# Optimization experiments

Measured on AMD Instinct MI355X. Metric: run time of the kernel, lower is better.

## Reference

```python
import jax, jax.numpy as jnp
import numpy as np

B, S, D, H = 2, 2048, 768, 12
DK = D // H


def setup_inputs() -> dict:
    key = jax.random.key(0)
    ks = jax.random.split(key, 10)
    sc = 0.02
    return {
        "k": jax.random.normal(ks[0], (B, S, D), jnp.float32),
        "q": jax.random.normal(ks[1], (B, S, D), jnp.float32),
        "v": jax.random.normal(ks[2], (B, S, D), jnp.float32),
        "mask": jnp.ones((B, 1, S, S), jnp.int32),
        "wq": jax.random.normal(ks[3], (D, D), jnp.float32) * sc,
        "bq": jnp.zeros((D,), jnp.float32),
        "wk": jax.random.normal(ks[4], (D, D), jnp.float32) * sc,
        "bk": jnp.zeros((D,), jnp.float32),
        "wv": jax.random.normal(ks[5], (D, D), jnp.float32) * sc,
        "bv": jnp.zeros((D,), jnp.float32),
        "wo": jax.random.normal(ks[6], (D, D), jnp.float32) * sc,
        "bo": jnp.zeros((D,), jnp.float32),
    }


def reference(k, q, v, mask, wq, bq, wk, bk, wv, bv, wo, bo):
    # Linear projections (torch Linear: x @ W^T + b)
    query = q @ wq.T + bq
    key_ = k @ wk.T + bk
    value = v @ wv.T + bv
    # [B,S,D] -> [B,H,S,DK]
    def split_heads(x):
        return x.reshape(B, S, H, DK).transpose(0, 2, 1, 3)
    Q, K, V = split_heads(query), split_heads(key_), split_heads(value)
    # NOTE: original masked_fill result is discarded -> mask is a no-op.
    scores = jnp.einsum("bhqd,bhkd->bhqk", Q, K) / jnp.sqrt(jnp.float32(DK))
    attn = jax.nn.softmax(scores, axis=-1)  # dropout p=0.0 -> identity
    out = jnp.einsum("bhqk,bhkd->bhqd", attn, V)
    out = out.transpose(0, 2, 1, 3).reshape(B, S, D)
    return out @ wo.T + bo
```

## Files before the change

### kernel.cpp

```cpp
#include <hip/hip_runtime.h>
#include <hip/hip_bf16.h>

#define B_  2
#define S_  2048
#define D_  768
#define H_  12
#define DK_ 64
#define NX_ (B_*S_*D_)
#define NW_ (D_*D_)
#define CSC 0.18033688011112042f

typedef __attribute__((ext_vector_type(8))) short  bf16x8;
typedef __attribute__((ext_vector_type(4))) float  f32x4;

__device__ __forceinline__ unsigned short f2bf(float f) {
    unsigned int u = __float_as_uint(f);
    u += 0x7fffu + ((u >> 16) & 1u);
    return (unsigned short)(u >> 16);
}

__device__ __forceinline__ unsigned pack_bf2(float a, float b) {
    const unsigned ua = __float_as_uint(a) + 0x8000u;
    const unsigned ub = __float_as_uint(b) + 0x8000u;
    return __builtin_amdgcn_perm(ub, ua, 0x07060302u);
}

__device__ __forceinline__ void async_cp16(const unsigned short* g,
                                           const unsigned short* lds_uniform_base) {
    __builtin_amdgcn_global_load_lds(
        (const __attribute__((address_space(1))) unsigned int*)(uintptr_t)g,
        (__attribute__((address_space(3))) unsigned int*)(unsigned int)(uintptr_t)lds_uniform_base,
        16, 0, 0);
}

struct CvtArgs { const float* s[7]; };

__global__ __launch_bounds__(256) void cvt_all(CvtArgs a,
                                               unsigned short* __restrict__ Xsw,
                                               unsigned short* __restrict__ Wsw) {
    const int bx = blockIdx.x;
    int y, inner;
    if (bx < 2304) { y = bx / 768;             inner = bx % 768; }
    else           { y = 3 + (bx - 2304) / 144; inner = (bx - 2304) % 144; }
    const int idx = inner * 256 + threadIdx.x;
    const int n  = idx / 48;
    const int g2 = idx % 48;
    const float* src = a.s[y] + (long)n * D_ + g2 * 16;
    const float zs = (y == 3) ? CSC : 1.0f;
    unsigned short o[16];
#pragma unroll
    for (int i = 0; i < 4; i++) {
        const float4 f = *(const float4*)(src + i * 4);
        o[i*4+0] = f2bf(f.x*zs); o[i*4+1] = f2bf(f.y*zs);
        o[i*4+2] = f2bf(f.z*zs); o[i*4+3] = f2bf(f.w*zs);
    }
    unsigned short* dst = (y >= 3) ? (Wsw + (long)(y - 3) * NW_ + (long)n * D_)
                                   : (Xsw + (long)y * NX_ + (long)n * D_);
    const int key = n & 7;
#pragma unroll
    for (int h = 0; h < 2; h++) {
        const int g8 = g2 * 2 + h;
        const int kdst = (g8 >> 3) * 64 + (((g8 & 7) ^ key) * 8);
        *(uint4*)(dst + kdst) = *(const uint4*)&o[h * 8];
    }
}

struct QkvArgs { const float* bias[3]; unsigned short* out[3]; };

__global__ __launch_bounds__(256, 3) void gemm_qkv(QkvArgs args,
                                                   const unsigned short* __restrict__ Xsw,
                                                   const unsigned short* __restrict__ Wsw) {
    __shared__ __align__(16) unsigned short smem[17408];
    unsigned short* As = smem;
    unsigned short* Bs = smem + 8192;

    const int t    = threadIdx.x;
    const int wave = t >> 6;
    const int lane = t & 63;
    const int l16  = lane & 15;
    const int quad = lane >> 4;
    const int wm   = wave >> 1, wn = wave & 1;
    const int m0   = blockIdx.x * 128;
    const int zz   = blockIdx.y / 6;
    const int nb   = blockIdx.y % 6;
    const int n0   = nb * 128;

    const unsigned short* Ap = Xsw + (long)zz * NX_;
    const unsigned short* Wp = Wsw + (long)zz * NW_;

    f32x4 acc[4][4];
#pragma unroll
    for (int s = 0; s < 4; s++)
#pragma unroll
        for (int j = 0; j < 4; j++) acc[s][j] = (f32x4){0.f, 0.f, 0.f, 0.f};

    const int lrow = lane >> 3;
    const int lcg  = lane & 7;

    for (int k0 = 0; k0 < D_; k0 += 64) {
        __syncthreads();
#pragma unroll
        for (int i = 0; i < 4; i++) {
            const int chunk = wave * 4 + i;
            async_cp16(Ap + (long)(m0 + chunk * 8 + lrow) * D_ + k0 + lcg * 8,
                       As + chunk * 512);
        }
#pragma unroll
        for (int i = 0; i < 4; i++) {
            const int chunk = wave * 4 + i;
            async_cp16(Wp + (long)(n0 + chunk * 8 + lrow) * D_ + k0 + lcg * 8,
                       Bs + chunk * 512);
        }
        __syncthreads();
#pragma unroll
        for (int ks = 0; ks < 2; ks++) {
            const int cg = ks * 4 + quad;
            bf16x8 af[4], bf[4];
#pragma unroll
            for (int s = 0; s < 4; s++) {
                const int r = wm * 64 + s * 16 + l16;
                af[s] = *(const bf16x8*)&As[r * 64 + ((cg ^ (r & 7)) * 8)];
            }
#pragma unroll
            for (int j = 0; j < 4; j++) {
                const int r = wn * 64 + j * 16 + l16;
                bf[j] = *(const bf16x8*)&Bs[r * 64 + ((cg ^ (r & 7)) * 8)];
            }
#pragma unroll
            for (int s = 0; s < 4; s++)
#pragma unroll
                for (int j = 0; j < 4; j++)
                    acc[s][j] = __builtin_amdgcn_mfma_f32_16x16x32_bf16(af[s], bf[j], acc[s][j], 0, 0, 0);
        }
    }
    __syncthreads();

    const int b     = m0 >> 11;
    const int sbase = m0 & (S_ - 1);
    const float zs  = (zz == 0) ? CSC : 1.0f;
    float bv[4];
#pragma unroll
    for (int j = 0; j < 4; j++) bv[j] = args.bias[zz][n0 + wn * 64 + j * 16 + l16] * zs;

    if (zz < 2) {
        unsigned short* Ls = smem;
#pragma unroll
        for (int s = 0; s < 4; s++)
#pragma unroll
            for (int j = 0; j < 4; j++)
#pragma unroll
                for (int r = 0; r < 4; r++)
                    Ls[(wm * 64 + s * 16 + quad * 4 + r) * 136 + wn * 64 + j * 16 + l16] =
                        f2bf(acc[s][j][r] + bv[j]);
        __syncthreads();
        const int row  = t >> 1;
        const int half = t & 1;
        unsigned short* Op = args.out[zz];
#pragma unroll
        for (int i = 0; i < 8; i++) {
            const int col  = half * 64 + i * 8;
            const int head = nb * 2 + half;
            const uint4 v = *(const uint4*)&Ls[row * 136 + col];
            *(uint4*)(Op + ((long)(b * H_ + head) * S_ + sbase + row) * DK_
                         + ((i ^ (row & 7)) * 8)) = v;
        }
    } else {
        unsigned short* Ls = smem;
#pragma unroll
        for (int s = 0; s < 4; s++)
#pragma unroll
            for (int j = 0; j < 4; j++)
#pragma unroll
                for (int r = 0; r < 4; r++) {
                    const int dk  = j * 16 + l16;
                    const int pos = wm * 64 + (quad * 4 + r) * 4 + s;
                    Ls[wn * 8704 + dk * 136 + pos] = f2bf(acc[s][j][r] + bv[j]);
                }
        __syncthreads();
        const int rowIdx = t >> 1;
        const int hh = rowIdx >> 6, dk = rowIdx & 63;
        const int half = t & 1;
        unsigned short* Op = args.out[2];
#pragma unroll
        for (int i = 0; i < 8; i++) {
            const int col = half * 64 + i * 8;
            const uint4 v = *(const uint4*)&Ls[hh * 8704 + dk * 136 + col];
            const int head = nb * 2 + hh;
            *(uint4*)(Op + ((long)(b * H_ + head) * DK_ + dk) * S_
                         + sbase + half * 64 + ((i ^ (dk & 7)) * 8)) = v;
        }
    }
}

__global__ __launch_bounds__(256, 3) void attn_kernel(
    const unsigned short* __restrict__ Q, const unsigned short* __restrict__ K,
    const unsigned short* __restrict__ Vt, unsigned short* __restrict__ Ao)
{
    const int t    = threadIdx.x;
    const int wave = t >> 6;
    const int lane = t & 63;
    const int l16  = lane & 15;
    const int quad = lane >> 4;
    const int bid  = blockIdx.x;
    const int bh    = bid % 24;
    const int qtile = bid / 24;

    const unsigned short* Qp = Q  + (long)bh * S_ * DK_;
    const unsigned short* Kp = K  + (long)bh * S_ * DK_;
    const unsigned short* Vp = Vt + (long)bh * DK_ * S_;

    __shared__ __align__(16) unsigned short smem[20480];
    unsigned short* Ps = smem + 16384;

    const int fkey = l16 & 7;
    const int fo0  = ((quad ^ fkey) * 8);
    const int fo1  = (((4 + quad) ^ fkey) * 8);

    bf16x8 qfrag[2];
    {
        const long qoff = (long)(qtile * 64 + wave * 16 + l16) * DK_;
        qfrag[0] = *(const bf16x8*)(Qp + qoff + fo0);
        qfrag[1] = *(const bf16x8*)(Qp + qoff + fo1);
    }

    const int ci0 = wave * 2;
    const int kd0 = ci0 * 512;
    const unsigned short* gk  = Kp + ci0 * 512 + lane * 8;
    const unsigned short* gv0 = Vp + (long)(ci0 * 8 + (lane >> 3)) * S_ + (lane & 7) * 8;
    const unsigned short* gv1 = gv0 + 8 * S_;

    async_cp16(gk,        smem + kd0);
    async_cp16(gk + 512,  smem + kd0 + 512);
    async_cp16(gv0,       smem + 8192 + kd0);
    async_cp16(gv1,       smem + 8192 + kd0 + 512);
    gk += 4096;  gv0 += 64;  gv1 += 64;

    f32x4 oacc[4];
#pragma unroll
    for (int j = 0; j < 4; j++) oacc[j] = (f32x4){0.f, 0.f, 0.f, 0.f};
    float lsum[4] = {0.f, 0.f, 0.f, 0.f};

    for (int it = 0; it < 32; ++it) {
        const int co = (it & 1) * 4096;
        const int no = 4096 - co;
        __syncthreads();
        const unsigned short* Ks = smem + co;
        const unsigned short* Vs = smem + 8192 + co;

        if (it < 31) {
            async_cp16(gk,        smem + no + kd0);
            async_cp16(gk + 512,  smem + no + kd0 + 512);
            async_cp16(gv0,       smem + 8192 + no + kd0);
            async_cp16(gv1,       smem + 8192 + no + kd0 + 512);
            gk += 4096;  gv0 += 64;  gv1 += 64;
        }

        f32x4 sacc[4];
#pragma unroll
        for (int j = 0; j < 4; j++) sacc[j] = (f32x4){0.f, 0.f, 0.f, 0.f};
#pragma unroll
        for (int ks = 0; ks < 2; ks++) {
            const int fo = ks ? fo1 : fo0;
            const bf16x8 qf = ks ? qfrag[1] : qfrag[0];
#pragma unroll
            for (int j = 0; j < 4; j++) {
                const bf16x8 bf = *(const bf16x8*)&Ks[(j * 16 + l16) * 64 + fo];
                sacc[j] = __builtin_amdgcn_mfma_f32_16x16x32_bf16(qf, bf, sacc[j], 0, 0, 0);
            }
        }

#pragma unroll
        for (int r = 0; r < 4; r++) {
            const float p0 = exp2f(sacc[0][r]);
            const float p1 = exp2f(sacc[1][r]);
            const float p2 = exp2f(sacc[2][r]);
            const float p3 = exp2f(sacc[3][r]);
            lsum[r] += (p0 + p1) + (p2 + p3);
            uint2 pk = {pack_bf2(p0, p1), pack_bf2(p2, p3)};
            const int prow = wave * 16 + quad * 4 + r;
            *(uint2*)&Ps[prow * 64 + (((l16 >> 1) ^ (prow & 7)) * 8) + (l16 & 1) * 4] = pk;
        }

#pragma unroll
        for (int ks = 0; ks < 2; ks++) {
            const int fo = ks ? fo1 : fo0;
            const bf16x8 pf = *(const bf16x8*)&Ps[(wave * 16 + l16) * 64 + fo];
#pragma unroll
            for (int j = 0; j < 4; j++) {
                const bf16x8 vf = *(const bf16x8*)&Vs[(j * 16 + l16) * 64 + fo];
                oacc[j] = __builtin_amdgcn_mfma_f32_16x16x32_bf16(pf, vf, oacc[j], 0, 0, 0);
            }
        }
    }

#pragma unroll
    for (int r = 0; r < 4; r++) {
#pragma unroll
        for (int off = 1; off < 16; off <<= 1)
            lsum[r] += __shfl_xor(lsum[r], off, 64);
        lsum[r] = 1.f / lsum[r];
    }

    __syncthreads();
#pragma unroll
    for (int j = 0; j < 4; j++)
#pragma unroll
        for (int r = 0; r < 4; r++) {
            const int row = wave * 16 + quad * 4 + r;
            const int c   = j * 2 + (l16 >> 3);
            Ps[row * 64 + ((c ^ (row & 7)) * 8) + (l16 & 7)] =
                f2bf(oacc[j][r] * lsum[r]);
        }

    const int b = bh / H_, h = bh % H_;
    const int row = t >> 2;
    const int p0  = (t & 3) * 2;
    const int qrow = qtile * 64 + row;
    unsigned short* dst = Ao + (long)(b * S_ + qrow) * D_ + h * DK_;
    *(uint4*)(dst + p0 * 8)       = *(const uint4*)&Ps[row * 64 + p0 * 8];
    *(uint4*)(dst + (p0 + 1) * 8) = *(const uint4*)&Ps[row * 64 + (p0 + 1) * 8];
}

__global__ __launch_bounds__(256, 4) void gemm_out(
    const unsigned short* __restrict__ A, const unsigned short* __restrict__ Wsw,
    const float* __restrict__ bias, float* __restrict__ Out)
{
    __shared__ __align__(16) unsigned short smem[8704];
    unsigned short* As = smem;
    unsigned short* Bs = smem + 4096;

    const int t    = threadIdx.x;
    const int wave = t >> 6;
    const int lane = t & 63;
    const int l16  = lane & 15;
    const int quad = lane >> 4;
    const int wm   = wave >> 1, wn = wave & 1;
    const int m0   = blockIdx.x * 64;
    const int n0   = blockIdx.y * 64;

    f32x4 acc[2][2];
#pragma unroll
    for (int s = 0; s < 2; s++)
#pragma unroll
        for (int j = 0; j < 2; j++) acc[s][j] = (f32x4){0.f, 0.f, 0.f, 0.f};

    const int lrow = lane >> 3;
    const int lcg  = lane & 7;

    for (int k0 = 0; k0 < D_; k0 += 64) {
        __syncthreads();
#pragma unroll
        for (int i = 0; i < 2; i++) {
            const int chunk = wave * 2 + i;
            async_cp16(A + (long)(m0 + chunk * 8 + lrow) * D_ + k0 + lcg * 8,
                       As + chunk * 512);
        }
#pragma unroll
        for (int i = 0; i < 2; i++) {
            const int chunk = wave * 2 + i;
            async_cp16(Wsw + (long)(n0 + chunk * 8 + lrow) * D_ + k0 + lcg * 8,
                       Bs + chunk * 512);
        }
        __syncthreads();
#pragma unroll
        for (int ks = 0; ks < 2; ks++) {
            const int cg = ks * 4 + quad;
            bf16x8 af[2], bf[2];
#pragma unroll
            for (int s = 0; s < 2; s++) {
                const int r = wm * 32 + s * 16 + l16;
                af[s] = *(const bf16x8*)&As[r * 64 + ((cg ^ (r & 7)) * 8)];
            }
#pragma unroll
            for (int j = 0; j < 2; j++) {
                const int r = wn * 32 + j * 16 + l16;
                bf[j] = *(const bf16x8*)&Bs[r * 64 + ((cg ^ (r & 7)) * 8)];
            }
#pragma unroll
            for (int s = 0; s < 2; s++)
#pragma unroll
                for (int j = 0; j < 2; j++)
                    acc[s][j] = __builtin_amdgcn_mfma_f32_16x16x32_bf16(af[s], bf[j], acc[s][j], 0, 0, 0);
        }
    }

    float bv[2];
#pragma unroll
    for (int j = 0; j < 2; j++) bv[j] = bias[n0 + wn * 32 + j * 16 + l16];

    __syncthreads();
    float* fl = (float*)smem;
#pragma unroll
    for (int s = 0; s < 2; s++)
#pragma unroll
        for (int j = 0; j < 2; j++)
#pragma unroll
            for (int r = 0; r < 4; r++)
                fl[(wm * 32 + s * 16 + quad * 4 + r) * 67 + wn * 32 + j * 16 + l16] =
                    acc[s][j][r] + bv[j];
    __syncthreads();
    const int row = t >> 2, c0 = (t & 3) * 16;
#pragma unroll
    for (int i = 0; i < 4; i++) {
        const float4 v = *(const float4*)&fl[row * 67 + c0 + i * 4];
        *(float4*)(Out + (long)(m0 + row) * D_ + n0 + c0 + i * 4) = v;
    }
}

extern "C" void kernel_launch(void* const* d_in, const int* in_sizes, int n_in,
                              void* d_out, int out_size, void* d_ws, size_t ws_size,
                              hipStream_t stream) {
    const float* k_in = (const float*)d_in[0];
    const float* q_in = (const float*)d_in[1];
    const float* v_in = (const float*)d_in[2];
    const float* wq = (const float*)d_in[4];
    const float* bq = (const float*)d_in[5];
    const float* wk = (const float*)d_in[6];
    const float* bk = (const float*)d_in[7];
    const float* wv = (const float*)d_in[8];
    const float* bv = (const float*)d_in[9];
    const float* wo = (const float*)d_in[10];
    const float* bo = (const float*)d_in[11];

    unsigned short* ws = (unsigned short*)d_ws;
    unsigned short* Wsw = ws;
    unsigned short* Qb  = Wsw + 4ll * NW_;
    unsigned short* Kb  = Qb + (long)NX_;
    unsigned short* Vt  = Kb + (long)NX_;
    unsigned short* Xsw = Vt + (long)NX_;
    unsigned short* Ao  = Xsw;

    CvtArgs ca;
    ca.s[0] = q_in; ca.s[1] = k_in; ca.s[2] = v_in;
    ca.s[3] = wq;   ca.s[4] = wk;   ca.s[5] = wv;  ca.s[6] = wo;
    cvt_all<<<dim3(2880), 256, 0, stream>>>(ca, Xsw, Wsw);

    QkvArgs qa;
    qa.bias[0] = bq; qa.bias[1] = bk; qa.bias[2] = bv;
    qa.out[0] = Qb;  qa.out[1] = Kb;  qa.out[2] = Vt;
    gemm_qkv<<<dim3(32, 18), 256, 0, stream>>>(qa, Xsw, Wsw);

    attn_kernel<<<dim3(768), 256, 0, stream>>>(Qb, Kb, Vt, Ao);

    gemm_out<<<dim3(64, 12), 256, 0, stream>>>(Ao, Wsw + 3ll * NW_, bo, (float*)d_out);
}
```

Measured before the change: 208.9 us.

## Keep attention probabilities in registers via transposed QK MFMA and V permutation

The QK^T MFMA operands are swapped so each lane holds a column of scores, and that layout matches the A-operand fragment of the PV MFMA. The probabilities are then packed to bf16 with v_cvt_pk_bf16_f32 and fed straight into the second MFMA, so the LDS round trip for P is gone. To keep the contraction consistent, the V-transpose writer in the projection kernel permutes the key positions. Row sums now come from two cross-quad shuffles plus a broadcast, and the LDS footprint drops. This relies on the custom position permutation in the V layout staying in step with the register order of P.

```diff
diff --git a/kernel.cpp b/kernel.cpp
--- a/kernel.cpp
+++ b/kernel.cpp
@@ -19,10 +19,10 @@
     return (unsigned short)(u >> 16);
 }
 
-__device__ __forceinline__ unsigned pack_bf2(float a, float b) {
-    const unsigned ua = __float_as_uint(a) + 0x8000u;
-    const unsigned ub = __float_as_uint(b) + 0x8000u;
-    return __builtin_amdgcn_perm(ub, ua, 0x07060302u);
+__device__ __forceinline__ unsigned cvtpk(float a, float b) {
+    unsigned r;
+    asm("v_cvt_pk_bf16_f32 %0, %1, %2" : "=v"(r) : "v"(a), "v"(b));
+    return r;
 }
 
 __device__ __forceinline__ void async_cp16(const unsigned short* g,
@@ -173,7 +173,7 @@
 #pragma unroll
                 for (int r = 0; r < 4; r++) {
                     const int dk  = j * 16 + l16;
-                    const int pos = wm * 64 + (quad * 4 + r) * 4 + s;
+                    const int pos = wm * 64 + (s >> 1) * 32 + quad * 8 + (s & 1) * 4 + r;
                     Ls[wn * 8704 + dk * 136 + pos] = f2bf(acc[s][j][r] + bv[j]);
                 }
         __syncthreads();
@@ -209,8 +209,7 @@
     const unsigned short* Kp = K  + (long)bh * S_ * DK_;
     const unsigned short* Vp = Vt + (long)bh * DK_ * S_;
 
-    __shared__ __align__(16) unsigned short smem[20480];
-    unsigned short* Ps = smem + 16384;
+    __shared__ __align__(16) unsigned short smem[16384];
 
     const int fkey = l16 & 7;
     const int fo0  = ((quad ^ fkey) * 8);
@@ -238,7 +237,7 @@
     f32x4 oacc[4];
 #pragma unroll
     for (int j = 0; j < 4; j++) oacc[j] = (f32x4){0.f, 0.f, 0.f, 0.f};
-    float lsum[4] = {0.f, 0.f, 0.f, 0.f};
+    float lsum = 0.f;
 
     for (int it = 0; it < 32; ++it) {
         const int co = (it & 1) * 4096;
@@ -265,26 +264,31 @@
 #pragma unroll
             for (int j = 0; j < 4; j++) {
                 const bf16x8 bf = *(const bf16x8*)&Ks[(j * 16 + l16) * 64 + fo];
-                sacc[j] = __builtin_amdgcn_mfma_f32_16x16x32_bf16(qf, bf, sacc[j], 0, 0, 0);
-            }
-        }
-
-#pragma unroll
-        for (int r = 0; r < 4; r++) {
-            const float p0 = exp2f(sacc[0][r]);
-            const float p1 = exp2f(sacc[1][r]);
-            const float p2 = exp2f(sacc[2][r]);
-            const float p3 = exp2f(sacc[3][r]);
-            lsum[r] += (p0 + p1) + (p2 + p3);
-            uint2 pk = {pack_bf2(p0, p1), pack_bf2(p2, p3)};
-            const int prow = wave * 16 + quad * 4 + r;
-            *(uint2*)&Ps[prow * 64 + (((l16 >> 1) ^ (prow & 7)) * 8) + (l16 & 1) * 4] = pk;
-        }
+                sacc[j] = __builtin_amdgcn_mfma_f32_16x16x32_bf16(bf, qf, sacc[j], 0, 0, 0);
+            }
+        }
+
+        float p[4][4];
+#pragma unroll
+        for (int j = 0; j < 4; j++)
+#pragma unroll
+            for (int r = 0; r < 4; r++)
+                p[j][r] = exp2f(sacc[j][r]);
+#pragma unroll
+        for (int j = 0; j < 4; j++)
+            lsum += (p[j][0] + p[j][1]) + (p[j][2] + p[j][3]);
+        uint4 pw0, pw1;
+        pw0.x = cvtpk(p[0][0], p[0][1]);  pw0.y = cvtpk(p[0][2], p[0][3]);
+        pw0.z = cvtpk(p[1][0], p[1][1]);  pw0.w = cvtpk(p[1][2], p[1][3]);
+        pw1.x = cvtpk(p[2][0], p[2][1]);  pw1.y = cvtpk(p[2][2], p[2][3]);
+        pw1.z = cvtpk(p[3][0], p[3][1]);  pw1.w = cvtpk(p[3][2], p[3][3]);
+        const bf16x8 pf0 = *(const bf16x8*)&pw0;
+        const bf16x8 pf1 = *(const bf16x8*)&pw1;
 
 #pragma unroll
         for (int ks = 0; ks < 2; ks++) {
             const int fo = ks ? fo1 : fo0;
-            const bf16x8 pf = *(const bf16x8*)&Ps[(wave * 16 + l16) * 64 + fo];
+            const bf16x8 pf = ks ? pf1 : pf0;
 #pragma unroll
             for (int j = 0; j < 4; j++) {
                 const bf16x8 vf = *(const bf16x8*)&Vs[(j * 16 + l16) * 64 + fo];
@@ -293,23 +297,23 @@
         }
     }
 
-#pragma unroll
-    for (int r = 0; r < 4; r++) {
-#pragma unroll
-        for (int off = 1; off < 16; off <<= 1)
-            lsum[r] += __shfl_xor(lsum[r], off, 64);
-        lsum[r] = 1.f / lsum[r];
-    }
+    lsum += __shfl_xor(lsum, 16, 64);
+    lsum += __shfl_xor(lsum, 32, 64);
+    const float inv = 1.f / lsum;
+    float scl[4];
+#pragma unroll
+    for (int r = 0; r < 4; r++) scl[r] = __shfl(inv, quad * 4 + r, 64);
 
     __syncthreads();
+    unsigned short* Sc = smem;
 #pragma unroll
     for (int j = 0; j < 4; j++)
 #pragma unroll
         for (int r = 0; r < 4; r++) {
             const int row = wave * 16 + quad * 4 + r;
             const int c   = j * 2 + (l16 >> 3);
-            Ps[row * 64 + ((c ^ (row & 7)) * 8) + (l16 & 7)] =
-                f2bf(oacc[j][r] * lsum[r]);
+            Sc[row * 64 + ((c ^ (row & 7)) * 8) + (l16 & 7)] =
+                f2bf(oacc[j][r] * scl[r]);
         }
 
     const int b = bh / H_, h = bh % H_;
@@ -317,8 +321,8 @@
     const int p0  = (t & 3) * 2;
     const int qrow = qtile * 64 + row;
     unsigned short* dst = Ao + (long)(b * S_ + qrow) * D_ + h * DK_;
-    *(uint4*)(dst + p0 * 8)       = *(const uint4*)&Ps[row * 64 + p0 * 8];
-    *(uint4*)(dst + (p0 + 1) * 8) = *(const uint4*)&Ps[row * 64 + (p0 + 1) * 8];
+    *(uint4*)(dst + p0 * 8)       = *(const uint4*)&Sc[row * 64 + p0 * 8];
+    *(uint4*)(dst + (p0 + 1) * 8) = *(const uint4*)&Sc[row * 64 + (p0 + 1) * 8];
 }
 
 __global__ __launch_bounds__(256, 4) void gemm_out(
```

Result: no change. 205.5 us (median of 2 runs) (-1.6%).
